# Kernel optimization log

Measured on AMD Instinct MI355X. Metric: run time of the kernel, lower is better.

## Reference

```python
import jax, jax.numpy as jnp
import numpy as np

NUM_EXPERTS = 8
HIDDEN = 2048
INTER = 1408
N_TOKENS = 8192


def setup_inputs() -> dict:
    key = jax.random.key(0)
    k1, k2, k3, k4, k5 = jax.random.split(key, 5)
    tokens = jax.random.normal(k1, (N_TOKENS, HIDDEN), dtype=jnp.float32)
    local_ids = jax.random.randint(k2, (N_TOKENS,), 0, NUM_EXPERTS)
    weights = jax.random.uniform(k3, (N_TOKENS,), dtype=jnp.float32)
    # kaiming_uniform-ish init scale
    bound1 = 1.0 / np.sqrt(HIDDEN)
    bound2 = 1.0 / np.sqrt(INTER)
    gate_up_proj = jax.random.uniform(k4, (NUM_EXPERTS, 2 * INTER, HIDDEN), dtype=jnp.float32, minval=-bound1, maxval=bound1)
    down_proj = jax.random.uniform(k5, (NUM_EXPERTS, HIDDEN, INTER), dtype=jnp.float32, minval=-bound2, maxval=bound2)
    return {"tokens": tokens, "local_ids": local_ids, "weights": weights,
            "gate_up_proj": gate_up_proj, "down_proj": down_proj}


def reference(tokens, local_ids, weights, gate_up_proj, down_proj):
    # tokens: [N, D]; local_ids: [N]; weights: [N]
    # gate_up_proj: [E, 2I, D]; down_proj: [E, D, I]
    E = gate_up_proj.shape[0]
    out = jnp.zeros_like(tokens)
    for e in range(E):  # fixed small expert loop; masked dense GEMMs
        fc1 = tokens @ gate_up_proj[e].T              # [N, 2I]
        gate, up = jnp.split(fc1, 2, axis=-1)         # SwiGLU convention: first half is gate
        h = jax.nn.silu(gate) * up                    # fused SiLU*up
        h = h * weights[:, None]                      # routing weight before down_proj
        o = h @ down_proj[e].T                        # [N, D]
        out = out + jnp.where((local_ids == e)[:, None], o, 0.0)
    return out
```

## Files before the change

### kernel.cpp

```cpp
#include <hip/hip_runtime.h>
#include <stdint.h>

#define E_    8
#define D_    2048
#define I_    1408
#define TWOI_ 2816
#define N_    8192
#define BM    128
#define MAXTILES 72
#define MPAD  9216

typedef __bf16 bf16x8 __attribute__((ext_vector_type(8)));
typedef float  floatx4 __attribute__((ext_vector_type(4)));

#define M_CNT   0
#define M_CUR   8
#define M_PB    16
#define M_NT    24
#define M_RTE   32
#define M_RTR   104
#define M_RTV   176

#define OFF_PERM  4096ULL
#define OFF_WPAD  40960ULL
#define OFF_APAD  81920ULL
#define OFF_HPAD  37830656ULL
#define OFF_GU    63782912ULL
#define OFF_DN    156057600ULL
#define WS_NEED   202194944ULL

__device__ inline void gload16(const void* g, void* lds) {
  __builtin_amdgcn_global_load_lds(
      (__attribute__((address_space(1))) void*)g,
      (__attribute__((address_space(3))) void*)lds, 16, 0, 0);
}

__device__ inline unsigned short f2bf(float f) {
  unsigned int u = __builtin_bit_cast(unsigned int, f);
  u += 0x7fffu + ((u >> 16) & 1u);
  return (unsigned short)(u >> 16);
}

__global__ void k_hist(const int* __restrict__ ids, int* meta) {
  int i = blockIdx.x * 256 + threadIdx.x;
  if (i < N_) atomicAdd(&meta[M_CNT + ids[i]], 1);
}

__global__ void k_meta(int* meta) {
  if (threadIdx.x != 0) return;
  int padr = 0, tiles = 0;
  for (int e = 0; e < E_; ++e) {
    meta[M_PB + e] = padr;
    int c = meta[M_CNT + e];
    int nt = (c + BM - 1) / BM;
    for (int t = 0; t < nt; ++t) {
      meta[M_RTE + tiles] = e;
      meta[M_RTR + tiles] = padr + t * BM;
      int v = c - t * BM; if (v > BM) v = BM;
      meta[M_RTV + tiles] = v;
      tiles++;
    }
    padr += nt * BM;
  }
  meta[M_NT] = tiles;
}

__global__ void k_scatter(const int* __restrict__ ids, const float* __restrict__ w,
                          int* meta, int* perm, float* wpad) {
  int i = blockIdx.x * 256 + threadIdx.x;
  if (i >= N_) return;
  int e = ids[i];
  int pos = atomicAdd(&meta[M_CUR + e], 1);
  int r = meta[M_PB + e] + pos;
  perm[r] = i;
  wpad[r] = w[i];
}

__global__ void k_gather(const float* __restrict__ tokens, const int* __restrict__ perm,
                         unsigned short* __restrict__ apad) {
  int r = blockIdx.x;
  int t = perm[r];
  if (t < 0) return;
  const float4* src = (const float4*)(tokens + (size_t)t * D_);
  uint4* dst = (uint4*)(apad + (size_t)r * D_);
  int i = threadIdx.x;
  float4 a = src[i * 2], b = src[i * 2 + 1];
  union { unsigned short s[8]; uint4 v; } pk;
  pk.s[0] = f2bf(a.x); pk.s[1] = f2bf(a.y); pk.s[2] = f2bf(a.z); pk.s[3] = f2bf(a.w);
  pk.s[4] = f2bf(b.x); pk.s[5] = f2bf(b.y); pk.s[6] = f2bf(b.z); pk.s[7] = f2bf(b.w);
  dst[i] = pk.v;
}

__global__ void k_cvt(const float* __restrict__ src, unsigned short* __restrict__ dst, int n8) {
  int i = blockIdx.x * 256 + threadIdx.x;
  if (i >= n8) return;
  const float4* s4 = (const float4*)src;
  float4 a = s4[i * 2], b = s4[i * 2 + 1];
  union { unsigned short s[8]; uint4 v; } pk;
  pk.s[0] = f2bf(a.x); pk.s[1] = f2bf(a.y); pk.s[2] = f2bf(a.z); pk.s[3] = f2bf(a.w);
  pk.s[4] = f2bf(b.x); pk.s[5] = f2bf(b.y); pk.s[6] = f2bf(b.z); pk.s[7] = f2bf(b.w);
  ((uint4*)dst)[i] = pk.v;
}

__global__ __launch_bounds__(256) void k_gemm1(
    const unsigned short* __restrict__ apad,
    const unsigned short* __restrict__ gub,
    const float* __restrict__ wpad,
    const int* __restrict__ meta,
    unsigned short* __restrict__ hpad) {
  int rt = blockIdx.x;
  if (rt >= meta[M_NT]) return;
  int ct = blockIdx.y;
  int e = meta[M_RTE + rt], row0 = meta[M_RTR + rt], nv = meta[M_RTV + rt];

  __shared__ __attribute__((aligned(16))) __bf16 As[BM * 32];
  __shared__ __attribute__((aligned(16))) __bf16 Bgs[64 * 32];
  __shared__ __attribute__((aligned(16))) __bf16 Bus[64 * 32];

  int tid = threadIdx.x;
  int lane = tid & 63;
  int wave = __builtin_amdgcn_readfirstlane(tid >> 6);

  const __bf16* A  = (const __bf16*)apad + (size_t)row0 * D_;
  const __bf16* Bg = (const __bf16*)gub + ((size_t)e * TWOI_ + (size_t)ct * 64) * D_;
  const __bf16* Bu = Bg + (size_t)I_ * D_;

  int srow = lane >> 2;
  int skq  = (lane & 3) * 8;

  floatx4 zero = {0.f, 0.f, 0.f, 0.f};
  floatx4 accg[2][4], accu[2][4];
#pragma unroll
  for (int mi = 0; mi < 2; ++mi)
#pragma unroll
    for (int ni = 0; ni < 4; ++ni) { accg[mi][ni] = zero; accu[mi][ni] = zero; }

  int quad8 = (lane >> 4) * 8;
  int l16 = lane & 15;

  for (int k0 = 0; k0 < D_; k0 += 32) {
    gload16(A + (size_t)(wave * 16 + srow) * D_ + k0 + skq, &As[(wave * 16) * 32]);
    gload16(A + (size_t)(64 + wave * 16 + srow) * D_ + k0 + skq, &As[(64 + wave * 16) * 32]);
    gload16(Bg + (size_t)(wave * 16 + srow) * D_ + k0 + skq, &Bgs[(wave * 16) * 32]);
    gload16(Bu + (size_t)(wave * 16 + srow) * D_ + k0 + skq, &Bus[(wave * 16) * 32]);
    __syncthreads();
    bf16x8 af[2], bg[4], bu[4];
#pragma unroll
    for (int mi = 0; mi < 2; ++mi)
      af[mi] = *(const bf16x8*)&As[(wave * 32 + mi * 16 + l16) * 32 + quad8];
#pragma unroll
    for (int ni = 0; ni < 4; ++ni) {
      bg[ni] = *(const bf16x8*)&Bgs[(ni * 16 + l16) * 32 + quad8];
      bu[ni] = *(const bf16x8*)&Bus[(ni * 16 + l16) * 32 + quad8];
    }
#pragma unroll
    for (int mi = 0; mi < 2; ++mi)
#pragma unroll
      for (int ni = 0; ni < 4; ++ni) {
        accg[mi][ni] = __builtin_amdgcn_mfma_f32_16x16x32_bf16(af[mi], bg[ni], accg[mi][ni], 0, 0, 0);
        accu[mi][ni] = __builtin_amdgcn_mfma_f32_16x16x32_bf16(af[mi], bu[ni], accu[mi][ni], 0, 0, 0);
      }
    __syncthreads();
  }

  int quad = lane >> 4;
#pragma unroll
  for (int mi = 0; mi < 2; ++mi)
#pragma unroll
    for (int reg = 0; reg < 4; ++reg) {
      int r = wave * 32 + mi * 16 + quad * 4 + reg;
      if (r < nv) {
        float wgt = wpad[row0 + r];
        unsigned short* hrow = hpad + (size_t)(row0 + r) * I_ + (size_t)ct * 64;
#pragma unroll
        for (int ni = 0; ni < 4; ++ni) {
          float g = accg[mi][ni][reg];
          float u = accu[mi][ni][reg];
          float s = g / (1.f + __expf(-g));
          hrow[ni * 16 + l16] = f2bf(s * u * wgt);
        }
      }
    }
}

__global__ __launch_bounds__(256) void k_gemm2(
    const unsigned short* __restrict__ hpad,
    const unsigned short* __restrict__ dnb,
    const int* __restrict__ meta,
    const int* __restrict__ perm,
    float* __restrict__ out) {
  int rt = blockIdx.x;
  if (rt >= meta[M_NT]) return;
  int ct = blockIdx.y;
  int e = meta[M_RTE + rt], row0 = meta[M_RTR + rt], nv = meta[M_RTV + rt];

  __shared__ __attribute__((aligned(16))) __bf16 As[128 * 32];
  __shared__ __attribute__((aligned(16))) __bf16 Bs[128 * 32];

  int tid = threadIdx.x;
  int lane = tid & 63;
  int wave = __builtin_amdgcn_readfirstlane(tid >> 6);
  int wm = wave >> 1, wn = wave & 1;

  const __bf16* A = (const __bf16*)hpad + (size_t)row0 * I_;
  const __bf16* B = (const __bf16*)dnb + ((size_t)e * D_ + (size_t)ct * 128) * I_;

  int srow = lane >> 2;
  int skq = (lane & 3) * 8;

  floatx4 zero = {0.f, 0.f, 0.f, 0.f};
  floatx4 acc[4][4];
#pragma unroll
  for (int mi = 0; mi < 4; ++mi)
#pragma unroll
    for (int ni = 0; ni < 4; ++ni) acc[mi][ni] = zero;

  int quad8 = (lane >> 4) * 8;
  int l16 = lane & 15;

  for (int k0 = 0; k0 < I_; k0 += 32) {
    gload16(A + (size_t)(wave * 16 + srow) * I_ + k0 + skq, &As[(wave * 16) * 32]);
    gload16(A + (size_t)(64 + wave * 16 + srow) * I_ + k0 + skq, &As[(64 + wave * 16) * 32]);
    gload16(B + (size_t)(wave * 16 + srow) * I_ + k0 + skq, &Bs[(wave * 16) * 32]);
    gload16(B + (size_t)(64 + wave * 16 + srow) * I_ + k0 + skq, &Bs[(64 + wave * 16) * 32]);
    __syncthreads();
    bf16x8 af[4], bfr[4];
#pragma unroll
    for (int mi = 0; mi < 4; ++mi)
      af[mi] = *(const bf16x8*)&As[(wm * 64 + mi * 16 + l16) * 32 + quad8];
#pragma unroll
    for (int ni = 0; ni < 4; ++ni)
      bfr[ni] = *(const bf16x8*)&Bs[(wn * 64 + ni * 16 + l16) * 32 + quad8];
#pragma unroll
    for (int mi = 0; mi < 4; ++mi)
#pragma unroll
      for (int ni = 0; ni < 4; ++ni)
        acc[mi][ni] = __builtin_amdgcn_mfma_f32_16x16x32_bf16(af[mi], bfr[ni], acc[mi][ni], 0, 0, 0);
    __syncthreads();
  }

  int quad = lane >> 4;
#pragma unroll
  for (int mi = 0; mi < 4; ++mi)
#pragma unroll
    for (int reg = 0; reg < 4; ++reg) {
      int r = wm * 64 + mi * 16 + quad * 4 + reg;
      if (r < nv) {
        int t = perm[row0 + r];
        float* orow = out + (size_t)t * D_ + (size_t)ct * 128 + wn * 64;
#pragma unroll
        for (int ni = 0; ni < 4; ++ni)
          orow[ni * 16 + l16] = acc[mi][ni][reg];
      }
    }
}

__global__ __launch_bounds__(256) void k_naive(
    const float* __restrict__ tokens, const int* __restrict__ ids,
    const float* __restrict__ w, const float* __restrict__ gu,
    const float* __restrict__ dn, float* __restrict__ out) {
  __shared__ float tok[D_];
  __shared__ float h[I_];
  int t = blockIdx.x;
  int e = ids[t];
  float wgt = w[t];
  for (int i = threadIdx.x; i < D_; i += 256) tok[i] = tokens[(size_t)t * D_ + i];
  __syncthreads();
  for (int j = threadIdx.x; j < I_; j += 256) {
    const float* wg = gu + ((size_t)e * TWOI_ + j) * D_;
    const float* wu = wg + (size_t)I_ * D_;
    float g = 0.f, u = 0.f;
    for (int k = 0; k < D_; ++k) { g += tok[k] * wg[k]; u += tok[k] * wu[k]; }
    h[j] = g / (1.f + __expf(-g)) * u * wgt;
  }
  __syncthreads();
  for (int d = threadIdx.x; d < D_; d += 256) {
    const float* wd = dn + ((size_t)e * D_ + d) * I_;
    float acc = 0.f;
    for (int k = 0; k < I_; ++k) acc += h[k] * wd[k];
    out[(size_t)t * D_ + d] = acc;
  }
}

extern "C" void kernel_launch(void* const* d_in, const int* in_sizes, int n_in,
                              void* d_out, int out_size, void* d_ws, size_t ws_size,
                              hipStream_t stream) {
  const float* tokens = (const float*)d_in[0];
  const int*   ids    = (const int*)d_in[1];
  const float* wts    = (const float*)d_in[2];
  const float* gu     = (const float*)d_in[3];
  const float* dn     = (const float*)d_in[4];
  float* out = (float*)d_out;

  if (ws_size < (size_t)WS_NEED) {
    k_naive<<<N_, 256, 0, stream>>>(tokens, ids, wts, gu, dn, out);
    return;
  }

  char* ws = (char*)d_ws;
  int* meta = (int*)ws;
  int* perm = (int*)(ws + OFF_PERM);
  float* wpad = (float*)(ws + OFF_WPAD);
  unsigned short* apad = (unsigned short*)(ws + OFF_APAD);
  unsigned short* hpad = (unsigned short*)(ws + OFF_HPAD);
  unsigned short* gub  = (unsigned short*)(ws + OFF_GU);
  unsigned short* dnb  = (unsigned short*)(ws + OFF_DN);

  hipMemsetAsync(meta, 0, 64, stream);
  hipMemsetAsync(perm, 0xFF, MPAD * 4, stream);
  k_hist<<<N_ / 256, 256, 0, stream>>>(ids, meta);
  k_meta<<<1, 1, 0, stream>>>(meta);
  k_scatter<<<N_ / 256, 256, 0, stream>>>(ids, wts, meta, perm, wpad);
  k_gather<<<MPAD, 256, 0, stream>>>(tokens, perm, apad);
  int ngu8 = E_ * TWOI_ * D_ / 8;
  int ndn8 = E_ * D_ * I_ / 8;
  k_cvt<<<(ngu8 + 255) / 256, 256, 0, stream>>>(gu, gub, ngu8);
  k_cvt<<<(ndn8 + 255) / 256, 256, 0, stream>>>(dn, dnb, ndn8);
  k_gemm1<<<dim3(MAXTILES, I_ / 64), 256, 0, stream>>>(apad, gub, wpad, meta, hpad);
  k_gemm2<<<dim3(MAXTILES, D_ / 128), 256, 0, stream>>>(hpad, dnb, meta, perm, out);
}
```

Measured before the change: 755.8 us.

## Use wave-aggregated atomics, grouped tile rasterization, and a K-64 step per sync in GEMMs

```diff
diff --git a/kernel.cpp b/kernel.cpp
--- a/kernel.cpp
+++ b/kernel.cpp
@@ -43,7 +43,12 @@
 
 __global__ void k_hist(const int* __restrict__ ids, int* meta) {
   int i = blockIdx.x * 256 + threadIdx.x;
-  if (i < N_) atomicAdd(&meta[M_CNT + ids[i]], 1);
+  int e = ids[i];
+  int lane = threadIdx.x & 63;
+  for (int ex = 0; ex < E_; ++ex) {
+    unsigned long long m = __ballot(e == ex);
+    if (lane == 0 && m) atomicAdd(&meta[M_CNT + ex], __popcll(m));
+  }
 }
 
 __global__ void k_meta(int* meta) {
@@ -68,12 +73,21 @@
 __global__ void k_scatter(const int* __restrict__ ids, const float* __restrict__ w,
                           int* meta, int* perm, float* wpad) {
   int i = blockIdx.x * 256 + threadIdx.x;
-  if (i >= N_) return;
   int e = ids[i];
-  int pos = atomicAdd(&meta[M_CUR + e], 1);
-  int r = meta[M_PB + e] + pos;
-  perm[r] = i;
-  wpad[r] = w[i];
+  float wv = w[i];
+  int lane = threadIdx.x & 63;
+  for (int ex = 0; ex < E_; ++ex) {
+    unsigned long long m = __ballot(e == ex);
+    if (!m) continue;
+    int base = 0;
+    if (lane == 0) base = atomicAdd(&meta[M_CUR + ex], __popcll(m));
+    base = __shfl(base, 0);
+    if (e == ex) {
+      int r = meta[M_PB + ex] + base + __popcll(m & ((1ULL << lane) - 1ULL));
+      perm[r] = i;
+      wpad[r] = wv;
+    }
+  }
 }
 
 __global__ void k_gather(const float* __restrict__ tokens, const int* __restrict__ perm,
@@ -108,14 +122,17 @@
     const float* __restrict__ wpad,
     const int* __restrict__ meta,
     unsigned short* __restrict__ hpad) {
-  int rt = blockIdx.x;
+  int bid = blockIdx.x;
+  int panel = bid / 176;
+  int rem = bid - panel * 176;
+  int ct = rem >> 3;
+  int rt = panel * 8 + (rem & 7);
   if (rt >= meta[M_NT]) return;
-  int ct = blockIdx.y;
   int e = meta[M_RTE + rt], row0 = meta[M_RTR + rt], nv = meta[M_RTV + rt];
 
-  __shared__ __attribute__((aligned(16))) __bf16 As[BM * 32];
-  __shared__ __attribute__((aligned(16))) __bf16 Bgs[64 * 32];
-  __shared__ __attribute__((aligned(16))) __bf16 Bus[64 * 32];
+  __shared__ __attribute__((aligned(16))) __bf16 As[2][BM * 32];
+  __shared__ __attribute__((aligned(16))) __bf16 Bgs[2][64 * 32];
+  __shared__ __attribute__((aligned(16))) __bf16 Bus[2][64 * 32];
 
   int tid = threadIdx.x;
   int lane = tid & 63;
@@ -138,28 +155,35 @@
   int quad8 = (lane >> 4) * 8;
   int l16 = lane & 15;
 
-  for (int k0 = 0; k0 < D_; k0 += 32) {
-    gload16(A + (size_t)(wave * 16 + srow) * D_ + k0 + skq, &As[(wave * 16) * 32]);
-    gload16(A + (size_t)(64 + wave * 16 + srow) * D_ + k0 + skq, &As[(64 + wave * 16) * 32]);
-    gload16(Bg + (size_t)(wave * 16 + srow) * D_ + k0 + skq, &Bgs[(wave * 16) * 32]);
-    gload16(Bu + (size_t)(wave * 16 + srow) * D_ + k0 + skq, &Bus[(wave * 16) * 32]);
+  for (int k0 = 0; k0 < D_; k0 += 64) {
+#pragma unroll
+    for (int p = 0; p < 2; ++p) {
+      int kk = k0 + p * 32;
+      gload16(A + (size_t)(wave * 16 + srow) * D_ + kk + skq, &As[p][(wave * 16) * 32]);
+      gload16(A + (size_t)(64 + wave * 16 + srow) * D_ + kk + skq, &As[p][(64 + wave * 16) * 32]);
+      gload16(Bg + (size_t)(wave * 16 + srow) * D_ + kk + skq, &Bgs[p][(wave * 16) * 32]);
+      gload16(Bu + (size_t)(wave * 16 + srow) * D_ + kk + skq, &Bus[p][(wave * 16) * 32]);
+    }
     __syncthreads();
-    bf16x8 af[2], bg[4], bu[4];
-#pragma unroll
-    for (int mi = 0; mi < 2; ++mi)
-      af[mi] = *(const bf16x8*)&As[(wave * 32 + mi * 16 + l16) * 32 + quad8];
-#pragma unroll
-    for (int ni = 0; ni < 4; ++ni) {
-      bg[ni] = *(const bf16x8*)&Bgs[(ni * 16 + l16) * 32 + quad8];
-      bu[ni] = *(const bf16x8*)&Bus[(ni * 16 + l16) * 32 + quad8];
-    }
-#pragma unroll
-    for (int mi = 0; mi < 2; ++mi)
+#pragma unroll
+    for (int p = 0; p < 2; ++p) {
+      bf16x8 af[2], bg[4], bu[4];
+#pragma unroll
+      for (int mi = 0; mi < 2; ++mi)
+        af[mi] = *(const bf16x8*)&As[p][(wave * 32 + mi * 16 + l16) * 32 + quad8];
 #pragma unroll
       for (int ni = 0; ni < 4; ++ni) {
-        accg[mi][ni] = __builtin_amdgcn_mfma_f32_16x16x32_bf16(af[mi], bg[ni], accg[mi][ni], 0, 0, 0);
-        accu[mi][ni] = __builtin_amdgcn_mfma_f32_16x16x32_bf16(af[mi], bu[ni], accu[mi][ni], 0, 0, 0);
+        bg[ni] = *(const bf16x8*)&Bgs[p][(ni * 16 + l16) * 32 + quad8];
+        bu[ni] = *(const bf16x8*)&Bus[p][(ni * 16 + l16) * 32 + quad8];
       }
+#pragma unroll
+      for (int mi = 0; mi < 2; ++mi)
+#pragma unroll
+        for (int ni = 0; ni < 4; ++ni) {
+          accg[mi][ni] = __builtin_amdgcn_mfma_f32_16x16x32_bf16(af[mi], bg[ni], accg[mi][ni], 0, 0, 0);
+          accu[mi][ni] = __builtin_amdgcn_mfma_f32_16x16x32_bf16(af[mi], bu[ni], accu[mi][ni], 0, 0, 0);
+        }
+    }
     __syncthreads();
   }
 
@@ -189,13 +213,16 @@
     const int* __restrict__ meta,
     const int* __restrict__ perm,
     float* __restrict__ out) {
-  int rt = blockIdx.x;
+  int bid = blockIdx.x;
+  int panel = bid / 128;
+  int rem = bid - panel * 128;
+  int ct = rem >> 3;
+  int rt = panel * 8 + (rem & 7);
   if (rt >= meta[M_NT]) return;
-  int ct = blockIdx.y;
   int e = meta[M_RTE + rt], row0 = meta[M_RTR + rt], nv = meta[M_RTV + rt];
 
-  __shared__ __attribute__((aligned(16))) __bf16 As[128 * 32];
-  __shared__ __attribute__((aligned(16))) __bf16 Bs[128 * 32];
+  __shared__ __attribute__((aligned(16))) __bf16 As[2][128 * 32];
+  __shared__ __attribute__((aligned(16))) __bf16 Bs[2][128 * 32];
 
   int tid = threadIdx.x;
   int lane = tid & 63;
@@ -218,24 +245,31 @@
   int quad8 = (lane >> 4) * 8;
   int l16 = lane & 15;
 
-  for (int k0 = 0; k0 < I_; k0 += 32) {
-    gload16(A + (size_t)(wave * 16 + srow) * I_ + k0 + skq, &As[(wave * 16) * 32]);
-    gload16(A + (size_t)(64 + wave * 16 + srow) * I_ + k0 + skq, &As[(64 + wave * 16) * 32]);
-    gload16(B + (size_t)(wave * 16 + srow) * I_ + k0 + skq, &Bs[(wave * 16) * 32]);
-    gload16(B + (size_t)(64 + wave * 16 + srow) * I_ + k0 + skq, &Bs[(64 + wave * 16) * 32]);
+  for (int k0 = 0; k0 < I_; k0 += 64) {
+#pragma unroll
+    for (int p = 0; p < 2; ++p) {
+      int kk = k0 + p * 32;
+      gload16(A + (size_t)(wave * 16 + srow) * I_ + kk + skq, &As[p][(wave * 16) * 32]);
+      gload16(A + (size_t)(64 + wave * 16 + srow) * I_ + kk + skq, &As[p][(64 + wave * 16) * 32]);
+      gload16(B + (size_t)(wave * 16 + srow) * I_ + kk + skq, &Bs[p][(wave * 16) * 32]);
+      gload16(B + (size_t)(64 + wave * 16 + srow) * I_ + kk + skq, &Bs[p][(64 + wave * 16) * 32]);
+    }
     __syncthreads();
-    bf16x8 af[4], bfr[4];
-#pragma unroll
-    for (int mi = 0; mi < 4; ++mi)
-      af[mi] = *(const bf16x8*)&As[(wm * 64 + mi * 16 + l16) * 32 + quad8];
-#pragma unroll
-    for (int ni = 0; ni < 4; ++ni)
-      bfr[ni] = *(const bf16x8*)&Bs[(wn * 64 + ni * 16 + l16) * 32 + quad8];
-#pragma unroll
-    for (int mi = 0; mi < 4; ++mi)
+#pragma unroll
+    for (int p = 0; p < 2; ++p) {
+      bf16x8 af[4], bfr[4];
+#pragma unroll
+      for (int mi = 0; mi < 4; ++mi)
+        af[mi] = *(const bf16x8*)&As[p][(wm * 64 + mi * 16 + l16) * 32 + quad8];
 #pragma unroll
       for (int ni = 0; ni < 4; ++ni)
-        acc[mi][ni] = __builtin_amdgcn_mfma_f32_16x16x32_bf16(af[mi], bfr[ni], acc[mi][ni], 0, 0, 0);
+        bfr[ni] = *(const bf16x8*)&Bs[p][(wn * 64 + ni * 16 + l16) * 32 + quad8];
+#pragma unroll
+      for (int mi = 0; mi < 4; ++mi)
+#pragma unroll
+        for (int ni = 0; ni < 4; ++ni)
+          acc[mi][ni] = __builtin_amdgcn_mfma_f32_16x16x32_bf16(af[mi], bfr[ni], acc[mi][ni], 0, 0, 0);
+    }
     __syncthreads();
   }
 
@@ -316,6 +350,6 @@
   int ndn8 = E_ * D_ * I_ / 8;
   k_cvt<<<(ngu8 + 255) / 256, 256, 0, stream>>>(gu, gub, ngu8);
   k_cvt<<<(ndn8 + 255) / 256, 256, 0, stream>>>(dn, dnb, ndn8);
-  k_gemm1<<<dim3(MAXTILES, I_ / 64), 256, 0, stream>>>(apad, gub, wpad, meta, hpad);
-  k_gemm2<<<dim3(MAXTILES, D_ / 128), 256, 0, stream>>>(hpad, dnb, meta, perm, out);
-}
+  k_gemm1<<<9 * 176, 256, 0, stream>>>(apad, gub, wpad, meta, hpad);
+  k_gemm2<<<9 * 128, 256, 0, stream>>>(hpad, dnb, meta, perm, out);
+}
```

Result: faster. 659.8 us (-12.7%).
